# Performance work log

Measured on AMD Instinct MI355X. Metric: run time of the kernel, lower is better.

## Reference

```python
import jax, jax.numpy as jnp
import numpy as np

B, NOTES, T, IN, H, NH = 32, 78, 128, 80, 128, 2  # batch, notes, time steps, input feats, time hidden, note hidden


def setup_inputs() -> dict:
    key = jax.random.key(0)
    ks = jax.random.split(key, 9)
    s = 0.1
    f32 = jnp.float32
    return {
        "x": jax.random.normal(ks[0], (B, NOTES, T, IN), f32),
        # time LSTM params (PyTorch layout: [4H, in], gate order i,f,g,o)
        "Wih_t": (jax.random.normal(ks[1], (4 * H, IN), f32) * s),
        "Whh_t": (jax.random.normal(ks[2], (4 * H, H), f32) * s),
        "bih_t": (jax.random.normal(ks[3], (4 * H,), f32) * s),
        "bhh_t": (jax.random.normal(ks[4], (4 * H,), f32) * s),
        # note LSTM params (hidden size 2)
        "Wih_n": (jax.random.normal(ks[5], (4 * NH, H), f32) * s),
        "Whh_n": (jax.random.normal(ks[6], (4 * NH, NH), f32) * s),
        "bih_n": (jax.random.normal(ks[7], (4 * NH,), f32) * s),
        "bhh_n": (jax.random.normal(ks[8], (4 * NH,), f32) * s),
    }


def _lstm(x, Wih, Whh, bih, bhh):
    # x: [N, L, in] -> all-step hidden states [N, L, H]; zero initial (h, c)
    N = x.shape[0]
    Hh = Whh.shape[1]
    b = bih + bhh

    def step(carry, xt):
        h, c = carry
        g = xt @ Wih.T + h @ Whh.T + b  # [N, 4H]
        i, f, gg, o = jnp.split(g, 4, axis=-1)
        c = jax.nn.sigmoid(f) * c + jax.nn.sigmoid(i) * jnp.tanh(gg)
        h = jax.nn.sigmoid(o) * jnp.tanh(c)
        return (h, c), h

    h0 = jnp.zeros((N, Hh), x.dtype)
    _, hs = jax.lax.scan(step, (h0, h0), x.transpose(1, 0, 2))  # hs: [L, N, H]
    return hs.transpose(1, 0, 2)


def reference(x, Wih_t, Whh_t, bih_t, bhh_t, Wih_n, Whh_n, bih_n, bhh_n):
    Bn = x.shape[0]
    # time LSTM: one sequence per (batch, note) -> batched into N = B*NOTES
    th = _lstm(x.reshape(Bn * NOTES, T, IN), Wih_t, Whh_t, bih_t, bhh_t)
    th = th.reshape(Bn, NOTES, T, H)
    # note LSTM: sequence over the 78-note axis at each time step -> batch B*T
    xn = th.transpose(0, 2, 1, 3).reshape(Bn * T, NOTES, H)
    nh = _lstm(xn, Wih_n, Whh_n, bih_n, bhh_n).reshape(Bn, T, NOTES, NH)
    return nh.reshape(Bn, T, NOTES * NH)  # [B, T, 156]
```

## Files before the change

kernel.cpp:

```cpp
#include <hip/hip_runtime.h>

#define B_     32
#define NOTES_ 78
#define T_     128
#define IN_    80
#define H_     128
#define NSEQ_  (B_*NOTES_)
#define MBLK   16
#define NBLK1  (NSEQ_/MBLK)
#define SEQ2_  (B_*T_)
#define XN8    (NSEQ_*T_*IN_/8)
#define SHSTR  136
#define SAXSTR 20

typedef __attribute__((ext_vector_type(8))) short short8;
typedef __attribute__((ext_vector_type(4))) float f32x4;

__device__ __forceinline__ unsigned short f2bf(float f) {
    unsigned u; __builtin_memcpy(&u, &f, 4);
    u += 0x7fffu + ((u >> 16) & 1u);
    return (unsigned short)(u >> 16);
}
__device__ __forceinline__ short8 pack8(const float* p) {
    short8 r;
    #pragma unroll
    for (int k = 0; k < 8; ++k) r[k] = (short)f2bf(p[k]);
    return r;
}
__device__ __forceinline__ float rcpf(float x)  { return __builtin_amdgcn_rcpf(x); }
__device__ __forceinline__ float sigm(float x)  { return rcpf(1.f + __expf(-x)); }
__device__ __forceinline__ float tanhr(float x) { return 2.f * rcpf(1.f + __expf(-2.f*x)) - 1.f; }

__global__ __launch_bounds__(256) void xcvt_kernel(
    const float* __restrict__ x, unsigned short* __restrict__ xb)
{
    const int i = blockIdx.x * 256 + threadIdx.x;
    if (i < XN8) {
        const f32x4 a = *(const f32x4*)(x + (size_t)i * 8);
        const f32x4 b = *(const f32x4*)(x + (size_t)i * 8 + 4);
        short8 r;
        #pragma unroll
        for (int k = 0; k < 4; ++k) { r[k] = (short)f2bf(a[k]); r[4+k] = (short)f2bf(b[k]); }
        *(short8*)(xb + (size_t)i * 8) = r;
    }
}


#define GN_TILE(TM1)                                                                   \
    if (wave == ((TM1) & 7)) {                                                         \
        short8 wnk[4];                                                                 \
        _Pragma("unroll")                                                              \
        for (int kt = 0; kt < 4; ++kt)                                                 \
            wnk[kt] = *(const short8*)(sWn + ((kt * 16 + m16) * 4 + quad) * 8);        \
        f32x4 an = (f32x4){0.f, 0.f, 0.f, 0.f};                                        \
        _Pragma("unroll")                                                              \
        for (int kt = 0; kt < 4; ++kt)                                                 \
            an = __builtin_amdgcn_mfma_f32_16x16x32_bf16(ah[kt], wnk[kt], an, 0, 0, 0);\
        if (m16 < 8) {                                                                 \
            _Pragma("unroll")                                                          \
            for (int r = 0; r < 4; ++r) {                                              \
                const int sq = seq0 + quad * 4 + r;                                    \
                const int bb = sq / NOTES_;                                            \
                const int nn = sq - bb * NOTES_;                                       \
                Gn[((unsigned)bb * (T_ * NOTES_) + (unsigned)nn) * 8u + (unsigned)m16  \
                   + (unsigned)(TM1) * (NOTES_ * 8)] = an[r] + bns;                    \
            }                                                                          \
        }                                                                              \
    }

template<bool XB16>
__global__ __launch_bounds__(768)
void time_lstm_kernel(
    const void* __restrict__ xin,
    const float* __restrict__ Wih,
    const float* __restrict__ Whh,
    const float* __restrict__ bih,
    const float* __restrict__ bhh,
    const float* __restrict__ Wn,
    const float* __restrict__ bn1,
    const float* __restrict__ bn2,
    float* __restrict__ Gn)
{
    __shared__ unsigned short sH[2][MBLK * SHSTR];
    __shared__ float sAx[2][512 * SAXSTR];
    __shared__ unsigned short sWn[4 * 16 * 4 * 8];

    const int tid  = threadIdx.x;
    const int wave = tid >> 6, lane = tid & 63;
    const int m16  = lane & 15, quad = lane >> 4;
    const int seq0 = blockIdx.x * MBLK;

    for (int i = tid; i < 2 * MBLK * SHSTR; i += 768)
        ((unsigned short*)sH)[i] = 0;
    for (int i = tid; i < 4 * 16 * 4 * 8; i += 768) {
        const int e = i & 7, qq = (i >> 3) & 3, m = (i >> 5) & 15, kt = i >> 9;
        sWn[i] = (m < 8) ? f2bf(Wn[m * H_ + kt * 32 + qq * 8 + e]) : (unsigned short)0;
    }

    const short8 zero8 = (short8){0,0,0,0,0,0,0,0};
    const float bns = (m16 < 8) ? (bn1[m16] + bn2[m16]) : 0.f;

    if (wave < 8) {
        const int j = wave * 16 + m16;

        short8 hf[4][4];
        #pragma unroll
        for (int g = 0; g < 4; ++g) {
            const int n = g * H_ + j;
            #pragma unroll
            for (int kt = 0; kt < 4; ++kt)
                hf[g][kt] = pack8(Whh + n * H_ + kt * 32 + quad * 8);
        }
        float cst[4] = {0.f, 0.f, 0.f, 0.f};

        __syncthreads();

        for (int t = 0; t < T_; ++t) {
            const unsigned short* sHr = sH[t & 1];
            unsigned short*       sHw = sH[(t & 1) ^ 1];
            const float*          axr = sAx[t & 1];

            short8 ah[4];
            #pragma unroll
            for (int kt = 0; kt < 4; ++kt)
                ah[kt] = *(const short8*)(sHr + m16 * SHSTR + kt * 32 + quad * 8);

            f32x4 acc[4];
            #pragma unroll
            for (int g = 0; g < 4; ++g)
                acc[g] = *(const f32x4*)(axr + (g * H_ + j) * SAXSTR + quad * 4);
            __builtin_amdgcn_s_setprio(1);
            #pragma unroll
            for (int g = 0; g < 4; ++g) {
                #pragma unroll
                for (int kt = 0; kt < 4; ++kt)
                    acc[g] = __builtin_amdgcn_mfma_f32_16x16x32_bf16(ah[kt], hf[g][kt], acc[g], 0, 0, 0);
            }
            __builtin_amdgcn_s_setprio(0);

            if (t > 0) GN_TILE(t - 1)

            float ei[4], ef[4], eg[4], eo[4];
            #pragma unroll
            for (int r = 0; r < 4; ++r) {
                ei[r] = __expf(-acc[0][r]);
                ef[r] = __expf(-acc[1][r]);
                eg[r] = __expf(-2.f * acc[2][r]);
                eo[r] = __expf(-acc[3][r]);
            }
            #pragma unroll
            for (int r = 0; r < 4; ++r) {
                const float di = 1.f + ei[r], df = 1.f + ef[r];
                const float dg = 1.f + eg[r], dd = 1.f + eo[r];
                const float s1 = di * df, s2 = dg * dd;
                const float R  = rcpf(s1 * s2);
                const float Rs2 = R * s2, Rs1 = R * s1;
                const float si = Rs2 * df;
                const float sf = Rs2 * di;
                const float so = Rs1 * dg;
                const float tg = 2.f * (Rs1 * dd) - 1.f;
                const float cf = sf * cst[r] + si * tg;
                cst[r] = cf;
                const float h = so * tanhr(cf);
                sHw[(quad * 4 + r) * SHSTR + j] = f2bf(h);
            }

            __builtin_amdgcn_sched_barrier(0);
            asm volatile("s_waitcnt lgkmcnt(0)" ::: "memory");
            __builtin_amdgcn_s_barrier();
            __builtin_amdgcn_sched_barrier(0);
        }

        {
            const unsigned short* sHr = sH[T_ & 1];
            short8 ah[4];
            #pragma unroll
            for (int kt = 0; kt < 4; ++kt)
                ah[kt] = *(const short8*)(sHr + m16 * SHSTR + kt * 32 + quad * 8);
            GN_TILE(T_ - 1)
        }
    } else {
        const int u = wave - 8;

        short8 wfh[8][3];
        float  bg8[8];
        #pragma unroll
        for (int nt = 0; nt < 8; ++nt) {
            const int n = u * H_ + nt * 16 + m16;
            #pragma unroll
            for (int kt = 0; kt < 3; ++kt) {
                const int k = kt * 32 + quad * 8;
                wfh[nt][kt] = (k < IN_) ? pack8(Wih + n * IN_ + k) : zero8;
            }
            bg8[nt] = bih[n] + bhh[n];
        }

        const float* xrf = XB16 ? nullptr
            : ((const float*)xin + (size_t)(seq0 + m16) * T_ * IN_);
        const unsigned short* xrb = XB16
            ? ((const unsigned short*)xin + (size_t)(seq0 + m16) * T_ * IN_) : nullptr;

        short8 ax0, ax1, ax2 = zero8;
        if (XB16) {
            const unsigned short* p = xrb;
            ax0 = *(const short8*)(p + quad * 8);
            ax1 = *(const short8*)(p + 32 + quad * 8);
            if (quad < 2) ax2 = *(const short8*)(p + 64 + quad * 8);
        } else {
            const float* p = xrf;
            ax0 = pack8(p + quad * 8);
            ax1 = pack8(p + 32 + quad * 8);
            if (quad < 2) ax2 = pack8(p + 64 + quad * 8);
        }
        {
            float* wp = sAx[0];
            #pragma unroll
            for (int nt = 0; nt < 8; ++nt) {
                f32x4 a8 = (f32x4){bg8[nt], bg8[nt], bg8[nt], bg8[nt]};
                a8 = __builtin_amdgcn_mfma_f32_16x16x32_bf16(ax0, wfh[nt][0], a8, 0, 0, 0);
                a8 = __builtin_amdgcn_mfma_f32_16x16x32_bf16(ax1, wfh[nt][1], a8, 0, 0, 0);
                a8 = __builtin_amdgcn_mfma_f32_16x16x32_bf16(ax2, wfh[nt][2], a8, 0, 0, 0);
                *(f32x4*)(wp + (u * H_ + nt * 16 + m16) * SAXSTR + quad * 4) = a8;
            }
        }
        if (XB16) {
            const unsigned short* p = xrb + IN_;
            ax0 = *(const short8*)(p + quad * 8);
            ax1 = *(const short8*)(p + 32 + quad * 8);
            if (quad < 2) ax2 = *(const short8*)(p + 64 + quad * 8);
        } else {
            const float* p = xrf + IN_;
            ax0 = pack8(p + quad * 8);
            ax1 = pack8(p + 32 + quad * 8);
            if (quad < 2) ax2 = pack8(p + 64 + quad * 8);
        }

        __syncthreads();

        for (int t = 0; t < T_; ++t) {
            if (t + 1 < T_) {
                float* wp = sAx[(t + 1) & 1];
                #pragma unroll
                for (int nt = 0; nt < 8; ++nt) {
                    f32x4 a8 = (f32x4){bg8[nt], bg8[nt], bg8[nt], bg8[nt]};
                    a8 = __builtin_amdgcn_mfma_f32_16x16x32_bf16(ax0, wfh[nt][0], a8, 0, 0, 0);
                    a8 = __builtin_amdgcn_mfma_f32_16x16x32_bf16(ax1, wfh[nt][1], a8, 0, 0, 0);
                    a8 = __builtin_amdgcn_mfma_f32_16x16x32_bf16(ax2, wfh[nt][2], a8, 0, 0, 0);
                    *(f32x4*)(wp + (u * H_ + nt * 16 + m16) * SAXSTR + quad * 4) = a8;
                }
            }
            if (t + 2 < T_) {
                if (XB16) {
                    const unsigned short* p = xrb + (t + 2) * IN_;
                    ax0 = *(const short8*)(p + quad * 8);
                    ax1 = *(const short8*)(p + 32 + quad * 8);
                    if (quad < 2) ax2 = *(const short8*)(p + 64 + quad * 8);
                } else {
                    const float* p = xrf + (t + 2) * IN_;
                    ax0 = pack8(p + quad * 8);
                    ax1 = pack8(p + 32 + quad * 8);
                    if (quad < 2) ax2 = pack8(p + 64 + quad * 8);
                }
            }

            __builtin_amdgcn_sched_barrier(0);
            asm volatile("s_waitcnt lgkmcnt(0)" ::: "memory");
            __builtin_amdgcn_s_barrier();
            __builtin_amdgcn_sched_barrier(0);
        }
    }
}

__global__ __launch_bounds__(64) void note_out_kernel(
    const float* __restrict__ Gn,
    const float* __restrict__ Whh,
    float* __restrict__ out)
{
    const int q = blockIdx.x * 64 + threadIdx.x;
    if (q >= SEQ2_) return;

    float w0[8], w1[8];
    #pragma unroll
    for (int g = 0; g < 8; ++g) { w0[g] = Whh[g * 2]; w1[g] = Whh[g * 2 + 1]; }

    const float* gp = Gn + (size_t)q * (NOTES_ * 8);
    float* op = out + (size_t)q * (NOTES_ * 2);

    float h0 = 0.f, h1 = 0.f, c0 = 0.f, c1 = 0.f;
    f32x4 ga = *(const f32x4*)(gp);
    f32x4 gb = *(const f32x4*)(gp + 4);
    for (int n = 0; n < NOTES_; ++n) {
        f32x4 na, nb;
        if (n + 1 < NOTES_) {
            na = *(const f32x4*)(gp + (n + 1) * 8);
            nb = *(const f32x4*)(gp + (n + 1) * 8 + 4);
        }
        const float i0 = ga[0] + w0[0] * h0 + w1[0] * h1;
        const float i1 = ga[1] + w0[1] * h0 + w1[1] * h1;
        const float f0 = ga[2] + w0[2] * h0 + w1[2] * h1;
        const float f1 = ga[3] + w0[3] * h0 + w1[3] * h1;
        const float g0 = gb[0] + w0[4] * h0 + w1[4] * h1;
        const float g1 = gb[1] + w0[5] * h0 + w1[5] * h1;
        const float o0 = gb[2] + w0[6] * h0 + w1[6] * h1;
        const float o1 = gb[3] + w0[7] * h0 + w1[7] * h1;
        c0 = sigm(f0) * c0 + sigm(i0) * tanhr(g0);
        c1 = sigm(f1) * c1 + sigm(i1) * tanhr(g1);
        h0 = sigm(o0) * tanhr(c0);
        h1 = sigm(o1) * tanhr(c1);
        op[n * 2 + 0] = h0;
        op[n * 2 + 1] = h1;
        ga = na; gb = nb;
    }
}

extern "C" void kernel_launch(void* const* d_in, const int* in_sizes, int n_in,
                              void* d_out, int out_size, void* d_ws, size_t ws_size,
                              hipStream_t stream) {
    const float* x     = (const float*)d_in[0];
    const float* Wih_t = (const float*)d_in[1];
    const float* Whh_t = (const float*)d_in[2];
    const float* bih_t = (const float*)d_in[3];
    const float* bhh_t = (const float*)d_in[4];
    const float* Wih_n = (const float*)d_in[5];
    const float* Whh_n = (const float*)d_in[6];
    const float* bih_n = (const float*)d_in[7];
    const float* bhh_n = (const float*)d_in[8];
    float* out = (float*)d_out;

    const size_t xb_bytes = (size_t)NSEQ_ * T_ * IN_ * 2;
    const size_t gn_bytes = (size_t)SEQ2_ * NOTES_ * 8 * 4;

    if (ws_size >= xb_bytes + gn_bytes) {
        unsigned short* xb = (unsigned short*)d_ws;
        float* Gn = (float*)((char*)d_ws + xb_bytes);
        xcvt_kernel<<<(XN8 + 255) / 256, 256, 0, stream>>>(x, xb);
        time_lstm_kernel<true><<<NBLK1, 768, 0, stream>>>(
            xb, Wih_t, Whh_t, bih_t, bhh_t, Wih_n, bih_n, bhh_n, Gn);
        note_out_kernel<<<SEQ2_ / 64, 64, 0, stream>>>(Gn, Whh_n, out);
    } else {
        float* Gn = (float*)d_ws;
        time_lstm_kernel<false><<<NBLK1, 768, 0, stream>>>(
            x, Wih_t, Whh_t, bih_t, bhh_t, Wih_n, bih_n, bhh_n, Gn);
        note_out_kernel<<<SEQ2_ / 64, 64, 0, stream>>>(Gn, Whh_n, out);
    }
}
```

Measured before the change: 354.3 us.

## Drop bf16 pre-convert kernel, note-major Gn layout, spread note kernel over more blocks

Removes the separate x-to-bf16 conversion pass and instead converts fp32 x to bf16 inside the time LSTM loader with vectorized f32x4 loads. Gn is transposed to a note-major layout so that consecutive note-recurrence threads read adjacent memory at each note step. The note kernel now runs 32 active lanes per block over 128 blocks instead of 64 over 64, and alternates two prefetch buffers. This avoids an extra global round trip through a bf16 copy of x, at the cost of twice the x bytes read inside the time kernel and half-empty wavefronts in the note kernel.

```diff
diff --git a/kernel.cpp b/kernel.cpp
--- a/kernel.cpp
+++ b/kernel.cpp
@@ -9,9 +9,9 @@
 #define MBLK   16
 #define NBLK1  (NSEQ_/MBLK)
 #define SEQ2_  (B_*T_)
-#define XN8    (NSEQ_*T_*IN_/8)
 #define SHSTR  136
 #define SAXSTR 20
+#define NSTR   (SEQ2_*8)
 
 typedef __attribute__((ext_vector_type(8))) short short8;
 typedef __attribute__((ext_vector_type(4))) float f32x4;
@@ -27,23 +27,15 @@
     for (int k = 0; k < 8; ++k) r[k] = (short)f2bf(p[k]);
     return r;
 }
+__device__ __forceinline__ short8 pack8v(f32x4 a, f32x4 b) {
+    short8 r;
+    #pragma unroll
+    for (int k = 0; k < 4; ++k) { r[k] = (short)f2bf(a[k]); r[4+k] = (short)f2bf(b[k]); }
+    return r;
+}
 __device__ __forceinline__ float rcpf(float x)  { return __builtin_amdgcn_rcpf(x); }
 __device__ __forceinline__ float sigm(float x)  { return rcpf(1.f + __expf(-x)); }
 __device__ __forceinline__ float tanhr(float x) { return 2.f * rcpf(1.f + __expf(-2.f*x)) - 1.f; }
-
-__global__ __launch_bounds__(256) void xcvt_kernel(
-    const float* __restrict__ x, unsigned short* __restrict__ xb)
-{
-    const int i = blockIdx.x * 256 + threadIdx.x;
-    if (i < XN8) {
-        const f32x4 a = *(const f32x4*)(x + (size_t)i * 8);
-        const f32x4 b = *(const f32x4*)(x + (size_t)i * 8 + 4);
-        short8 r;
-        #pragma unroll
-        for (int k = 0; k < 4; ++k) { r[k] = (short)f2bf(a[k]); r[4+k] = (short)f2bf(b[k]); }
-        *(short8*)(xb + (size_t)i * 8) = r;
-    }
-}
 
 
 #define GN_TILE(TM1)                                                                   \
@@ -62,16 +54,27 @@
                 const int sq = seq0 + quad * 4 + r;                                    \
                 const int bb = sq / NOTES_;                                            \
                 const int nn = sq - bb * NOTES_;                                       \
-                Gn[((unsigned)bb * (T_ * NOTES_) + (unsigned)nn) * 8u + (unsigned)m16  \
-                   + (unsigned)(TM1) * (NOTES_ * 8)] = an[r] + bns;                    \
+                Gn[((unsigned)nn * SEQ2_ + (unsigned)bb * T_ + (unsigned)(TM1)) * 8u   \
+                   + (unsigned)m16] = an[r] + bns;                                     \
             }                                                                          \
         }                                                                              \
     }
 
-template<bool XB16>
+#define LOADX(T)                                                                       \
+    {                                                                                  \
+        const float* p = xrf + (size_t)(T) * IN_;                                      \
+        ax0 = pack8v(*(const f32x4*)(p + quad * 8),                                    \
+                     *(const f32x4*)(p + quad * 8 + 4));                               \
+        ax1 = pack8v(*(const f32x4*)(p + 32 + quad * 8),                               \
+                     *(const f32x4*)(p + 32 + quad * 8 + 4));                          \
+        if (quad < 2)                                                                  \
+            ax2 = pack8v(*(const f32x4*)(p + 64 + quad * 8),                           \
+                         *(const f32x4*)(p + 64 + quad * 8 + 4));                      \
+    }
+
 __global__ __launch_bounds__(768)
 void time_lstm_kernel(
-    const void* __restrict__ xin,
+    const float* __restrict__ x,
     const float* __restrict__ Wih,
     const float* __restrict__ Whh,
     const float* __restrict__ bih,
@@ -195,23 +198,10 @@
             bg8[nt] = bih[n] + bhh[n];
         }
 
-        const float* xrf = XB16 ? nullptr
-            : ((const float*)xin + (size_t)(seq0 + m16) * T_ * IN_);
-        const unsigned short* xrb = XB16
-            ? ((const unsigned short*)xin + (size_t)(seq0 + m16) * T_ * IN_) : nullptr;
+        const float* xrf = x + (size_t)(seq0 + m16) * T_ * IN_;
 
         short8 ax0, ax1, ax2 = zero8;
-        if (XB16) {
-            const unsigned short* p = xrb;
-            ax0 = *(const short8*)(p + quad * 8);
-            ax1 = *(const short8*)(p + 32 + quad * 8);
-            if (quad < 2) ax2 = *(const short8*)(p + 64 + quad * 8);
-        } else {
-            const float* p = xrf;
-            ax0 = pack8(p + quad * 8);
-            ax1 = pack8(p + 32 + quad * 8);
-            if (quad < 2) ax2 = pack8(p + 64 + quad * 8);
-        }
+        LOADX(0)
         {
             float* wp = sAx[0];
             #pragma unroll
@@ -223,17 +213,7 @@
                 *(f32x4*)(wp + (u * H_ + nt * 16 + m16) * SAXSTR + quad * 4) = a8;
             }
         }
-        if (XB16) {
-            const unsigned short* p = xrb + IN_;
-            ax0 = *(const short8*)(p + quad * 8);
-            ax1 = *(const short8*)(p + 32 + quad * 8);
-            if (quad < 2) ax2 = *(const short8*)(p + 64 + quad * 8);
-        } else {
-            const float* p = xrf + IN_;
-            ax0 = pack8(p + quad * 8);
-            ax1 = pack8(p + 32 + quad * 8);
-            if (quad < 2) ax2 = pack8(p + 64 + quad * 8);
-        }
+        LOADX(1)
 
         __syncthreads();
 
@@ -249,19 +229,7 @@
                     *(f32x4*)(wp + (u * H_ + nt * 16 + m16) * SAXSTR + quad * 4) = a8;
                 }
             }
-            if (t + 2 < T_) {
-                if (XB16) {
-                    const unsigned short* p = xrb + (t + 2) * IN_;
-                    ax0 = *(const short8*)(p + quad * 8);
-                    ax1 = *(const short8*)(p + 32 + quad * 8);
-                    if (quad < 2) ax2 = *(const short8*)(p + 64 + quad * 8);
-                } else {
-                    const float* p = xrf + (t + 2) * IN_;
-                    ax0 = pack8(p + quad * 8);
-                    ax1 = pack8(p + 32 + quad * 8);
-                    if (quad < 2) ax2 = pack8(p + 64 + quad * 8);
-                }
-            }
+            if (t + 2 < T_) LOADX(t + 2)
 
             __builtin_amdgcn_sched_barrier(0);
             asm volatile("s_waitcnt lgkmcnt(0)" ::: "memory");
@@ -276,41 +244,55 @@
     const float* __restrict__ Whh,
     float* __restrict__ out)
 {
-    const int q = blockIdx.x * 64 + threadIdx.x;
-    if (q >= SEQ2_) return;
+    const int lane = threadIdx.x;
+    if (lane >= 32) return;
+    const int q = blockIdx.x * 32 + lane;
 
     float w0[8], w1[8];
     #pragma unroll
     for (int g = 0; g < 8; ++g) { w0[g] = Whh[g * 2]; w1[g] = Whh[g * 2 + 1]; }
 
-    const float* gp = Gn + (size_t)q * (NOTES_ * 8);
+    const float* gp = Gn + (size_t)q * 8;
     float* op = out + (size_t)q * (NOTES_ * 2);
 
     float h0 = 0.f, h1 = 0.f, c0 = 0.f, c1 = 0.f;
-    f32x4 ga = *(const f32x4*)(gp);
-    f32x4 gb = *(const f32x4*)(gp + 4);
-    for (int n = 0; n < NOTES_; ++n) {
-        f32x4 na, nb;
-        if (n + 1 < NOTES_) {
-            na = *(const f32x4*)(gp + (n + 1) * 8);
-            nb = *(const f32x4*)(gp + (n + 1) * 8 + 4);
-        }
-        const float i0 = ga[0] + w0[0] * h0 + w1[0] * h1;
-        const float i1 = ga[1] + w0[1] * h0 + w1[1] * h1;
-        const float f0 = ga[2] + w0[2] * h0 + w1[2] * h1;
-        const float f1 = ga[3] + w0[3] * h0 + w1[3] * h1;
-        const float g0 = gb[0] + w0[4] * h0 + w1[4] * h1;
-        const float g1 = gb[1] + w0[5] * h0 + w1[5] * h1;
-        const float o0 = gb[2] + w0[6] * h0 + w1[6] * h1;
-        const float o1 = gb[3] + w0[7] * h0 + w1[7] * h1;
-        c0 = sigm(f0) * c0 + sigm(i0) * tanhr(g0);
-        c1 = sigm(f1) * c1 + sigm(i1) * tanhr(g1);
-        h0 = sigm(o0) * tanhr(c0);
-        h1 = sigm(o1) * tanhr(c1);
-        op[n * 2 + 0] = h0;
-        op[n * 2 + 1] = h1;
-        ga = na; gb = nb;
-    }
+
+    f32x4 gaA = *(const f32x4*)(gp);
+    f32x4 gbA = *(const f32x4*)(gp + 4);
+    f32x4 gaB = *(const f32x4*)(gp + NSTR);
+    f32x4 gbB = *(const f32x4*)(gp + NSTR + 4);
+
+#define NOTE_BODY(GA, GB, N)                                                   \
+    {                                                                          \
+        const float i0 = GA[0] + w0[0] * h0 + w1[0] * h1;                      \
+        const float i1 = GA[1] + w0[1] * h0 + w1[1] * h1;                      \
+        const float f0 = GA[2] + w0[2] * h0 + w1[2] * h1;                      \
+        const float f1 = GA[3] + w0[3] * h0 + w1[3] * h1;                      \
+        const float g0 = GB[0] + w0[4] * h0 + w1[4] * h1;                      \
+        const float g1 = GB[1] + w0[5] * h0 + w1[5] * h1;                      \
+        const float o0 = GB[2] + w0[6] * h0 + w1[6] * h1;                      \
+        const float o1 = GB[3] + w0[7] * h0 + w1[7] * h1;                      \
+        c0 = sigm(f0) * c0 + sigm(i0) * tanhr(g0);                             \
+        c1 = sigm(f1) * c1 + sigm(i1) * tanhr(g1);                             \
+        h0 = sigm(o0) * tanhr(c0);                                             \
+        h1 = sigm(o1) * tanhr(c1);                                             \
+        op[(N) * 2 + 0] = h0;                                                  \
+        op[(N) * 2 + 1] = h1;                                                  \
+    }
+
+    for (int n = 0; n < NOTES_; n += 2) {
+        NOTE_BODY(gaA, gbA, n)
+        if (n + 2 < NOTES_) {
+            gaA = *(const f32x4*)(gp + (size_t)(n + 2) * NSTR);
+            gbA = *(const f32x4*)(gp + (size_t)(n + 2) * NSTR + 4);
+        }
+        NOTE_BODY(gaB, gbB, n + 1)
+        if (n + 3 < NOTES_) {
+            gaB = *(const f32x4*)(gp + (size_t)(n + 3) * NSTR);
+            gbB = *(const f32x4*)(gp + (size_t)(n + 3) * NSTR + 4);
+        }
+    }
+#undef NOTE_BODY
 }
 
 extern "C" void kernel_launch(void* const* d_in, const int* in_sizes, int n_in,
@@ -327,20 +309,8 @@
     const float* bhh_n = (const float*)d_in[8];
     float* out = (float*)d_out;
 
-    const size_t xb_bytes = (size_t)NSEQ_ * T_ * IN_ * 2;
-    const size_t gn_bytes = (size_t)SEQ2_ * NOTES_ * 8 * 4;
-
-    if (ws_size >= xb_bytes + gn_bytes) {
-        unsigned short* xb = (unsigned short*)d_ws;
-        float* Gn = (float*)((char*)d_ws + xb_bytes);
-        xcvt_kernel<<<(XN8 + 255) / 256, 256, 0, stream>>>(x, xb);
-        time_lstm_kernel<true><<<NBLK1, 768, 0, stream>>>(
-            xb, Wih_t, Whh_t, bih_t, bhh_t, Wih_n, bih_n, bhh_n, Gn);
-        note_out_kernel<<<SEQ2_ / 64, 64, 0, stream>>>(Gn, Whh_n, out);
-    } else {
-        float* Gn = (float*)d_ws;
-        time_lstm_kernel<false><<<NBLK1, 768, 0, stream>>>(
-            x, Wih_t, Whh_t, bih_t, bhh_t, Wih_n, bih_n, bhh_n, Gn);
-        note_out_kernel<<<SEQ2_ / 64, 64, 0, stream>>>(Gn, Whh_n, out);
-    }
-}
+    float* Gn = (float*)d_ws;
+    time_lstm_kernel<<<NBLK1, 768, 0, stream>>>(
+        x, Wih_t, Whh_t, bih_t, bhh_t, Wih_n, bih_n, bhh_n, Gn);
+    note_out_kernel<<<128, 64, 0, stream>>>(Gn, Whh_n, out);
+}
```

New measurement: 438.5 us. +23.8%, slower.

## Fuse fp32-to-bf16 input conversion into time LSTM with deferred packing

Applied to the files above, without the earlier changes.

Drops the separate xcvt kernel that wrote a bf16 copy of x to workspace. The time LSTM kernel now reads fp32 x directly, issuing the loads for step t+2 as raw f32x4 registers and packing them to bf16 only just before use in the next iteration, so load latency overlaps the barrier and recurrence. This removes one kernel launch and the extra write and re-read of the converted input. In exchange it reads twice the bytes per step inside the latency-critical loop and holds more registers live.

```diff
diff --git a/kernel.cpp b/kernel.cpp
--- a/kernel.cpp
+++ b/kernel.cpp
@@ -9,7 +9,6 @@
 #define MBLK   16
 #define NBLK1  (NSEQ_/MBLK)
 #define SEQ2_  (B_*T_)
-#define XN8    (NSEQ_*T_*IN_/8)
 #define SHSTR  136
 #define SAXSTR 20
 
@@ -27,23 +26,15 @@
     for (int k = 0; k < 8; ++k) r[k] = (short)f2bf(p[k]);
     return r;
 }
+__device__ __forceinline__ short8 pack8v(f32x4 a, f32x4 b) {
+    short8 r;
+    #pragma unroll
+    for (int k = 0; k < 4; ++k) { r[k] = (short)f2bf(a[k]); r[4+k] = (short)f2bf(b[k]); }
+    return r;
+}
 __device__ __forceinline__ float rcpf(float x)  { return __builtin_amdgcn_rcpf(x); }
 __device__ __forceinline__ float sigm(float x)  { return rcpf(1.f + __expf(-x)); }
 __device__ __forceinline__ float tanhr(float x) { return 2.f * rcpf(1.f + __expf(-2.f*x)) - 1.f; }
-
-__global__ __launch_bounds__(256) void xcvt_kernel(
-    const float* __restrict__ x, unsigned short* __restrict__ xb)
-{
-    const int i = blockIdx.x * 256 + threadIdx.x;
-    if (i < XN8) {
-        const f32x4 a = *(const f32x4*)(x + (size_t)i * 8);
-        const f32x4 b = *(const f32x4*)(x + (size_t)i * 8 + 4);
-        short8 r;
-        #pragma unroll
-        for (int k = 0; k < 4; ++k) { r[k] = (short)f2bf(a[k]); r[4+k] = (short)f2bf(b[k]); }
-        *(short8*)(xb + (size_t)i * 8) = r;
-    }
-}
 
 
 #define GN_TILE(TM1)                                                                   \
@@ -68,10 +59,28 @@
         }                                                                              \
     }
 
-template<bool XB16>
+#define ISSUEX(T)                                                                      \
+    {                                                                                  \
+        const float* p = xrf + (size_t)(T) * IN_;                                      \
+        fx0a = *(const f32x4*)(p + quad * 8);                                          \
+        fx0b = *(const f32x4*)(p + quad * 8 + 4);                                      \
+        fx1a = *(const f32x4*)(p + 32 + quad * 8);                                     \
+        fx1b = *(const f32x4*)(p + 32 + quad * 8 + 4);                                 \
+        if (quad < 2) {                                                                \
+            fx2a = *(const f32x4*)(p + 64 + quad * 8);                                 \
+            fx2b = *(const f32x4*)(p + 64 + quad * 8 + 4);                             \
+        }                                                                              \
+    }
+#define PACKX                                                                          \
+    {                                                                                  \
+        ax0 = pack8v(fx0a, fx0b);                                                      \
+        ax1 = pack8v(fx1a, fx1b);                                                      \
+        if (quad < 2) ax2 = pack8v(fx2a, fx2b);                                        \
+    }
+
 __global__ __launch_bounds__(768)
 void time_lstm_kernel(
-    const void* __restrict__ xin,
+    const float* __restrict__ x,
     const float* __restrict__ Wih,
     const float* __restrict__ Whh,
     const float* __restrict__ bih,
@@ -195,23 +204,14 @@
             bg8[nt] = bih[n] + bhh[n];
         }
 
-        const float* xrf = XB16 ? nullptr
-            : ((const float*)xin + (size_t)(seq0 + m16) * T_ * IN_);
-        const unsigned short* xrb = XB16
-            ? ((const unsigned short*)xin + (size_t)(seq0 + m16) * T_ * IN_) : nullptr;
-
+        const float* xrf = x + (size_t)(seq0 + m16) * T_ * IN_;
+
+        f32x4 zf = (f32x4){0.f, 0.f, 0.f, 0.f};
+        f32x4 fx0a = zf, fx0b = zf, fx1a = zf, fx1b = zf, fx2a = zf, fx2b = zf;
         short8 ax0, ax1, ax2 = zero8;
-        if (XB16) {
-            const unsigned short* p = xrb;
-            ax0 = *(const short8*)(p + quad * 8);
-            ax1 = *(const short8*)(p + 32 + quad * 8);
-            if (quad < 2) ax2 = *(const short8*)(p + 64 + quad * 8);
-        } else {
-            const float* p = xrf;
-            ax0 = pack8(p + quad * 8);
-            ax1 = pack8(p + 32 + quad * 8);
-            if (quad < 2) ax2 = pack8(p + 64 + quad * 8);
-        }
+
+        ISSUEX(0)
+        PACKX
         {
             float* wp = sAx[0];
             #pragma unroll
@@ -223,22 +223,13 @@
                 *(f32x4*)(wp + (u * H_ + nt * 16 + m16) * SAXSTR + quad * 4) = a8;
             }
         }
-        if (XB16) {
-            const unsigned short* p = xrb + IN_;
-            ax0 = *(const short8*)(p + quad * 8);
-            ax1 = *(const short8*)(p + 32 + quad * 8);
-            if (quad < 2) ax2 = *(const short8*)(p + 64 + quad * 8);
-        } else {
-            const float* p = xrf + IN_;
-            ax0 = pack8(p + quad * 8);
-            ax1 = pack8(p + 32 + quad * 8);
-            if (quad < 2) ax2 = pack8(p + 64 + quad * 8);
-        }
+        ISSUEX(1)
 
         __syncthreads();
 
         for (int t = 0; t < T_; ++t) {
             if (t + 1 < T_) {
+                PACKX
                 float* wp = sAx[(t + 1) & 1];
                 #pragma unroll
                 for (int nt = 0; nt < 8; ++nt) {
@@ -249,19 +240,7 @@
                     *(f32x4*)(wp + (u * H_ + nt * 16 + m16) * SAXSTR + quad * 4) = a8;
                 }
             }
-            if (t + 2 < T_) {
-                if (XB16) {
-                    const unsigned short* p = xrb + (t + 2) * IN_;
-                    ax0 = *(const short8*)(p + quad * 8);
-                    ax1 = *(const short8*)(p + 32 + quad * 8);
-                    if (quad < 2) ax2 = *(const short8*)(p + 64 + quad * 8);
-                } else {
-                    const float* p = xrf + (t + 2) * IN_;
-                    ax0 = pack8(p + quad * 8);
-                    ax1 = pack8(p + 32 + quad * 8);
-                    if (quad < 2) ax2 = pack8(p + 64 + quad * 8);
-                }
-            }
+            if (t + 2 < T_) ISSUEX(t + 2)
 
             __builtin_amdgcn_sched_barrier(0);
             asm volatile("s_waitcnt lgkmcnt(0)" ::: "memory");
@@ -327,20 +306,8 @@
     const float* bhh_n = (const float*)d_in[8];
     float* out = (float*)d_out;
 
-    const size_t xb_bytes = (size_t)NSEQ_ * T_ * IN_ * 2;
-    const size_t gn_bytes = (size_t)SEQ2_ * NOTES_ * 8 * 4;
-
-    if (ws_size >= xb_bytes + gn_bytes) {
-        unsigned short* xb = (unsigned short*)d_ws;
-        float* Gn = (float*)((char*)d_ws + xb_bytes);
-        xcvt_kernel<<<(XN8 + 255) / 256, 256, 0, stream>>>(x, xb);
-        time_lstm_kernel<true><<<NBLK1, 768, 0, stream>>>(
-            xb, Wih_t, Whh_t, bih_t, bhh_t, Wih_n, bih_n, bhh_n, Gn);
-        note_out_kernel<<<SEQ2_ / 64, 64, 0, stream>>>(Gn, Whh_n, out);
-    } else {
-        float* Gn = (float*)d_ws;
-        time_lstm_kernel<false><<<NBLK1, 768, 0, stream>>>(
-            x, Wih_t, Whh_t, bih_t, bhh_t, Wih_n, bih_n, bhh_n, Gn);
-        note_out_kernel<<<SEQ2_ / 64, 64, 0, stream>>>(Gn, Whh_n, out);
-    }
-}
+    float* Gn = (float*)d_ws;
+    time_lstm_kernel<<<NBLK1, 768, 0, stream>>>(
+        x, Wih_t, Whh_t, bih_t, bhh_t, Wih_n, bih_n, bhh_n, Gn);
+    note_out_kernel<<<SEQ2_ / 64, 64, 0, stream>>>(Gn, Whh_n, out);
+}
```

Result: slower. 384.4 us (+8.5%).
